# Kernel optimization log

Hardware: AMD Instinct MI355X
Metric: run time of the kernel (lower is better)

The kernel has to match this reference:

```python
import jax, jax.numpy as jnp
import numpy as np

H = 16  # num_heads
B, N, M, D = 4, 512, 2048, 1024
FF = 4096  # mlp_ratio * D
LN_EPS = 1e-5


def _ln(x, g, b):
    m = x.mean(-1, keepdims=True)
    v = ((x - m) ** 2).mean(-1, keepdims=True)
    return (x - m) * jax.lax.rsqrt(v + LN_EPS) * g + b


def _attn(q_in, k_in, v_in, wq, bq, wk, bk, wv, bv, wp, bp):
    b, n, d = q_in.shape
    m = k_in.shape[1]
    hd = d // H
    scale = hd ** -0.5
    q = (q_in @ wq + bq).reshape(b, n, H, hd) * scale
    k = (k_in @ wk + bk).reshape(b, m, H, hd)
    v = (v_in @ wv + bv).reshape(b, m, H, hd)
    attn = jax.nn.softmax(jnp.einsum('bnhd,bmhd->bhnm', q, k), axis=-1)
    out = jnp.einsum('bhnm,bmhd->bnhd', attn, v).reshape(b, n, d)
    return out @ wp + bp


def setup_inputs() -> dict:
    key = jax.random.key(0)
    ks = iter(jax.random.split(key, 32))
    rnd = lambda shape: jax.random.normal(next(ks), shape, dtype=jnp.float32)
    w = lambda *shape: rnd(shape) * 0.02
    inp = {
        'state': rnd((B, N, D)),
        'patches': rnd((B, M, D)),
        'patches_pos_embed': rnd((B, M, D)),
        'state_query': rnd((B, N, D)),
    }
    for p in ('ca', 'sa'):
        inp[f'{p}_wq'] = w(D, D); inp[f'{p}_bq'] = jnp.zeros((D,), jnp.float32)
        inp[f'{p}_wk'] = w(D, D); inp[f'{p}_bk'] = jnp.zeros((D,), jnp.float32)
        inp[f'{p}_wv'] = w(D, D); inp[f'{p}_bv'] = jnp.zeros((D,), jnp.float32)
        inp[f'{p}_wp'] = w(D, D); inp[f'{p}_bp'] = jnp.zeros((D,), jnp.float32)
    inp['w1'] = w(D, FF); inp['b1'] = jnp.zeros((FF,), jnp.float32)
    inp['w2'] = w(FF, D); inp['b2'] = jnp.zeros((D,), jnp.float32)
    for i in (1, 2, 3):
        inp[f'n{i}_g'] = jnp.ones((D,), jnp.float32)
        inp[f'n{i}_b'] = jnp.zeros((D,), jnp.float32)
        inp[f'ls{i}'] = jnp.full((D,), 1e-5, jnp.float32)
    return inp


def reference(state, patches, patches_pos_embed, state_query,
              ca_wq, ca_bq, ca_wk, ca_bk, ca_wv, ca_bv, ca_wp, ca_bp,
              sa_wq, sa_bq, sa_wk, sa_bk, sa_wv, sa_bv, sa_wp, sa_bp,
              w1, b1, w2, b2,
              n1_g, n1_b, n2_g, n2_b, n3_g, n3_b,
              ls1, ls2, ls3):
    # pre-norm path of TransformerLayer.forward_pre (dropouts/drop_path = 0)
    state = state + state_query
    kv = patches + patches_pos_embed
    cross = _attn(_ln(state, n1_g, n1_b), kv, patches,
                  ca_wq, ca_bq, ca_wk, ca_bk, ca_wv, ca_bv, ca_wp, ca_bp)
    state = state + cross * ls1
    ns = _ln(state, n2_g, n2_b)
    selfa = _attn(ns, ns, ns,
                  sa_wq, sa_bq, sa_wk, sa_bk, sa_wv, sa_bv, sa_wp, sa_bp)
    state = state + selfa * ls2
    h = jax.nn.gelu(_ln(state, n3_g, n3_b) @ w1 + b1)
    return state + (h @ w2 + b2) * ls3
```

## Files before the change

### kernel.cpp

```cpp
#include <hip/hip_runtime.h>

#define DEV __device__ __forceinline__

typedef __bf16 bf16x8 __attribute__((ext_vector_type(8)));
typedef float f32x4 __attribute__((ext_vector_type(4)));

DEV unsigned short f2bf(float f) {
  __bf16 h = (__bf16)f;
  return __builtin_bit_cast(unsigned short, h);
}
DEV unsigned int cvtpk(float lo, float hi) {
  unsigned int r;
  asm("v_cvt_pk_bf16_f32 %0, %1, %2" : "=v"(r) : "v"(lo), "v"(hi));
  return r;
}

DEV void gload16(const void* g, void* l) {
  __builtin_amdgcn_global_load_lds(
      (const __attribute__((address_space(1))) unsigned int*)g,
      (__attribute__((address_space(3))) unsigned int*)l, 16, 0, 0);
}

DEV void tconv64_body(const float* __restrict__ W, unsigned short* __restrict__ Wt,
                      int K, int N, int bx, int by) {
  __shared__ float tile[64][65];
  const int t = threadIdx.x;
  const int rr = t >> 4;
  const int cc = (t & 15) * 4;
#pragma unroll
  for (int it = 0; it < 4; it++) {
    float4 v = *reinterpret_cast<const float4*>(
        &W[(size_t)(by * 64 + it * 16 + rr) * N + bx * 64 + cc]);
    tile[it * 16 + rr][cc] = v.x;
    tile[it * 16 + rr][cc + 1] = v.y;
    tile[it * 16 + rr][cc + 2] = v.z;
    tile[it * 16 + rr][cc + 3] = v.w;
  }
  __syncthreads();
  const int nr = t >> 3;
  const int kc = (t & 7) * 8;
#pragma unroll
  for (int it = 0; it < 2; it++) {
    const int n = it * 32 + nr;
    uint4 o;
    o.x = cvtpk(tile[kc + 0][n], tile[kc + 1][n]);
    o.y = cvtpk(tile[kc + 2][n], tile[kc + 3][n]);
    o.z = cvtpk(tile[kc + 4][n], tile[kc + 5][n]);
    o.w = cvtpk(tile[kc + 6][n], tile[kc + 7][n]);
    *reinterpret_cast<uint4*>(&Wt[(size_t)(bx * 64 + n) * K + by * 64 + kc]) = o;
  }
}

DEV void add_ln_body(const float* __restrict__ a, const float* b, float* x0_out,
                     unsigned short* __restrict__ y, const float* __restrict__ gam,
                     const float* __restrict__ bet, int row) {
  const int t = threadIdx.x;
  const int c = t * 4;
  const size_t base = (size_t)row * 1024 + c;
  float4 v = *reinterpret_cast<const float4*>(a + base);
  if (b) {
    float4 v2 = *reinterpret_cast<const float4*>(b + base);
    v.x += v2.x; v.y += v2.y; v.z += v2.z; v.w += v2.w;
  }
  if (x0_out) *reinterpret_cast<float4*>(x0_out + base) = v;
  float s = v.x + v.y + v.z + v.w;
  float sq = v.x * v.x + v.y * v.y + v.z * v.z + v.w * v.w;
#pragma unroll
  for (int o = 32; o > 0; o >>= 1) {
    s += __shfl_xor(s, o);
    sq += __shfl_xor(sq, o);
  }
  __shared__ float ps[4], pq[4];
  const int w = t >> 6;
  if ((t & 63) == 0) { ps[w] = s; pq[w] = sq; }
  __syncthreads();
  s = ps[0] + ps[1] + ps[2] + ps[3];
  sq = pq[0] + pq[1] + pq[2] + pq[3];
  const float mean = s * (1.f / 1024.f);
  const float var = sq * (1.f / 1024.f) - mean * mean;
  const float rstd = rsqrtf(var + 1e-5f);
  float4 gv = *reinterpret_cast<const float4*>(gam + c);
  float4 bv = *reinterpret_cast<const float4*>(bet + c);
  uint2 o2;
  o2.x = cvtpk((v.x - mean) * rstd * gv.x + bv.x, (v.y - mean) * rstd * gv.y + bv.y);
  o2.y = cvtpk((v.z - mean) * rstd * gv.z + bv.z, (v.w - mean) * rstd * gv.w + bv.w);
  *reinterpret_cast<uint2*>(y + base) = o2;
}

DEV void kvcast_body(const float* __restrict__ p, const float* __restrict__ pe,
                     unsigned short* __restrict__ kvo, unsigned short* __restrict__ po,
                     int bid) {
  const size_t i = ((size_t)bid * 256 + threadIdx.x) * 4;
  float4 a = *reinterpret_cast<const float4*>(p + i);
  float4 b = *reinterpret_cast<const float4*>(pe + i);
  uint2 kv2, p2;
  kv2.x = cvtpk(a.x + b.x, a.y + b.y);
  kv2.y = cvtpk(a.z + b.z, a.w + b.w);
  p2.x = cvtpk(a.x, a.y);
  p2.y = cvtpk(a.z, a.w);
  *reinterpret_cast<uint2*>(kvo + i) = kv2;
  *reinterpret_cast<uint2*>(po + i) = p2;
}

struct Pre {
  const float* sqw[8]; unsigned short* sqd[8];
  const float* w1; unsigned short* w1t;
  const float* w2; unsigned short* w2t;
  const float* state; const float* squery; float* stateF; unsigned short* lnB;
  const float* n1_g; const float* n1_b;
  const float* patches; const float* ppe; unsigned short* kvB; unsigned short* patB;
  const float* bq; const float* bk; const float* bv; float* bqkv;
};
__global__ __launch_bounds__(256) void prelude_kernel(Pre p) {
  const int bid = blockIdx.x;
  if (bid < 8192) {
    kvcast_body(p.patches, p.ppe, p.kvB, p.patB, bid);
  } else if (bid < 10240) {
    const int i = bid - 8192;
    const int m = i >> 8, wi = i & 255;
    tconv64_body(p.sqw[m], p.sqd[m], 1024, 1024, wi & 15, wi >> 4);
  } else if (bid < 11264) {
    const int i = bid - 10240;
    tconv64_body(p.w1, p.w1t, 1024, 4096, i & 63, i >> 6);
  } else if (bid < 12288) {
    const int i = bid - 11264;
    tconv64_body(p.w2, p.w2t, 4096, 1024, i & 15, i >> 4);
  } else if (bid < 14336) {
    add_ln_body(p.state, p.squery, p.stateF, p.lnB, p.n1_g, p.n1_b, bid - 12288);
  } else {
    const int i = (bid - 14336) * 256 + threadIdx.x;
    p.bqkv[i] = i < 1024 ? p.bq[i] : (i < 2048 ? p.bk[i - 1024] : p.bv[i - 2048]);
  }
}

__global__ __launch_bounds__(256) void add_ln_kernel(
    const float* __restrict__ a, const float* b, float* x0_out,
    unsigned short* __restrict__ y, const float* __restrict__ gam,
    const float* __restrict__ bet) {
  add_ln_body(a, b, x0_out, y, gam, bet, blockIdx.x);
}

DEV void xcd_swizzle(int gx, int gy, int& bx, int& by, int& bz) {
  const int gxy = gx * gy;
  const int nwg = gxy * gridDim.z;
  const int orig = (blockIdx.z * gy + blockIdx.y) * gx + blockIdx.x;
  const int q = nwg >> 3, r = nwg & 7;
  const int xcd = orig & 7;
  int wgid = (xcd < r ? xcd * (q + 1) : r * (q + 1) + (xcd - r) * q) + (orig >> 3);
  bz = wgid / gxy;
  wgid -= bz * gxy;
  if (gy >= gx) { by = wgid / gx; bx = wgid - by * gx; }
  else          { bx = wgid / gy; by = wgid - bx * gy; }
}

template <int BM, int BN>
DEV void gemm_core(const unsigned short* __restrict__ A,
                   const unsigned short* __restrict__ Bt,
                   unsigned short* As, unsigned short* Bs,
                   int brow, int bcol, int K, int lda, int koff,
                   f32x4 (&acc)[BM / 32][BN / 32]) {
  constexpr int WM = BM / 32, WN = BN / 32;
  const int t = threadIdx.x;
  const int lane = t & 63, w = t >> 6;
  const int wr = w >> 1, wc = w & 1;
  const int g = lane >> 4, lr = lane & 15;
  const int srow = lane >> 2, scol = (lane & 3) * 8;

  auto stage = [&](int buf, int k0) {
#pragma unroll
    for (int i = 0; i < BM / 64; i++) {
      const int r0 = (i * 4 + w) * 16;
      gload16(A + (size_t)(brow + r0 + srow) * lda + koff + k0 + scol,
              &As[buf * BM * 32 + r0 * 32]);
    }
#pragma unroll
    for (int i = 0; i < BN / 64; i++) {
      const int r0 = (i * 4 + w) * 16;
      gload16(Bt + (size_t)(bcol + r0 + srow) * lda + koff + k0 + scol,
              &Bs[buf * BN * 32 + r0 * 32]);
    }
  };

  stage(0, 0);
  const int nk = K / 32;
  int cur = 0;
  for (int kt = 0; kt < nk; kt++) {
    __syncthreads();
    if (kt + 1 < nk) stage(cur ^ 1, (kt + 1) * 32);
    bf16x8 af[WM], bfr[WN];
#pragma unroll
    for (int m = 0; m < WM; m++)
      af[m] = *reinterpret_cast<const bf16x8*>(
          &As[cur * BM * 32 + (wr * (BM / 2) + m * 16 + lr) * 32 + g * 8]);
#pragma unroll
    for (int n = 0; n < WN; n++)
      bfr[n] = *reinterpret_cast<const bf16x8*>(
          &Bs[cur * BN * 32 + (wc * (BN / 2) + n * 16 + lr) * 32 + g * 8]);
    __builtin_amdgcn_s_setprio(1);
#pragma unroll
    for (int m = 0; m < WM; m++)
#pragma unroll
      for (int n = 0; n < WN; n++)
        acc[m][n] = __builtin_amdgcn_mfma_f32_16x16x32_bf16(af[m], bfr[n], acc[m][n], 0, 0, 0);
    __builtin_amdgcn_s_setprio(0);
    cur ^= 1;
  }
}

template <int BM, int BN>
DEV void epilogue_vT(f32x4 (&acc)[BM / 32][BN / 32], unsigned short* smem,
                     unsigned short* __restrict__ vT, const float* __restrict__ bias,
                     int brow, int bcol, int vcol0, int vNk, int rpb) {
  constexpr int WM = BM / 32, WN = BN / 32;
  constexpr int LDT = 136;
  const int t = threadIdx.x, lane = t & 63, w = t >> 6;
  const int wr = w >> 1, wc = w & 1;
  const int g = lane >> 4, lr = lane & 15;
  __syncthreads();
#pragma unroll
  for (int m = 0; m < WM; m++) {
    const int row0 = wr * (BM / 2) + m * 16 + g * 4;
#pragma unroll
    for (int n = 0; n < WN; n++) {
      const int cc = wc * (BN / 2) + n * 16 + lr;
      const float bv = bias[bcol + cc];
      uint2 pk;
      pk.x = cvtpk(acc[m][n][0] + bv, acc[m][n][1] + bv);
      pk.y = cvtpk(acc[m][n][2] + bv, acc[m][n][3] + bv);
      *reinterpret_cast<uint2*>(&smem[cc * LDT + row0]) = pk;
    }
  }
  __syncthreads();
  const int b = brow / rpb;
  const int kvb = brow % rpb;
  constexpr int ITERS = BM * BN / (256 * 8);
#pragma unroll
  for (int it = 0; it < ITERS; it++) {
    const int idx = it * 256 + t;
    const int cc = idx / (BM / 8);
    const int ch = idx % (BM / 8);
    const int dg = bcol + cc - vcol0;
    const int h = dg >> 6, d = dg & 63;
    uint4 v = *reinterpret_cast<uint4*>(&smem[cc * LDT + ch * 8]);
    *reinterpret_cast<uint4*>(
        &vT[((size_t)(b * 16 + h) * 64 + d) * vNk + kvb + ch * 8]) = v;
  }
}

template <int EPI, int BM, int BN>
__global__ __launch_bounds__(256) void gemm_kernel(
    const unsigned short* __restrict__ A, const unsigned short* __restrict__ Bt,
    const float* __restrict__ bias, const float* resid,
    const float* __restrict__ ls, void* outp, int M, int N, int K, int lda,
    unsigned short* vT, int vcol0, int vNk, int rpb) {
  constexpr int WM = BM / 32;
  constexpr int WN = BN / 32;
  constexpr int STG = 2 * BM * 32 + 2 * BN * 32;
  constexpr int TRN = BN * 136;
  constexpr int SME = (EPI == 5 && TRN > STG) ? TRN : STG;
  __shared__ __align__(16) unsigned short smem[SME];
  unsigned short* As = smem;
  unsigned short* Bs = smem + 2 * BM * 32;
  const int t = threadIdx.x;
  const int lane = t & 63, w = t >> 6;
  const int wr = w >> 1, wc = w & 1;
  const int g = lane >> 4, lr = lane & 15;

  int bx, by, bz;
  xcd_swizzle(gridDim.x, gridDim.y, bx, by, bz);
  const int brow = by * BM, bcol = bx * BN;

  f32x4 acc[WM][WN] = {};
  gemm_core<BM, BN>(A, Bt, As, Bs, brow, bcol, K, lda, bz * K, acc);

  if (EPI == 5 && bcol >= vcol0) {
    epilogue_vT<BM, BN>(acc, smem, vT, bias, brow, bcol, vcol0, vNk, rpb);
    return;
  }

#pragma unroll
  for (int m = 0; m < WM; m++) {
    const int row0 = brow + wr * (BM / 2) + m * 16 + g * 4;
#pragma unroll
    for (int n = 0; n < WN; n++) {
      const int col = bcol + wc * (BN / 2) + n * 16 + lr;
      const float bv = (EPI == 4) ? 0.f : bias[col];
#pragma unroll
      for (int r = 0; r < 4; r++) {
        const float v = acc[m][n][r] + bv;
        const size_t idx = (size_t)(row0 + r) * N + col;
        if (EPI == 0 || EPI == 5) {
          ((unsigned short*)outp)[idx] = f2bf(v);
        } else if (EPI == 2) {
          ((float*)outp)[idx] = resid[idx] + v * ls[col];
        } else if (EPI == 3) {
          const float tth = tanhf(0.7978845608028654f * (v + 0.044715f * v * v * v));
          ((unsigned short*)outp)[idx] = f2bf(0.5f * v * (1.f + tth));
        } else {
          ((float*)outp)[(size_t)bz * M * N + idx] = v;
        }
      }
    }
  }
}

struct G3 {
  const unsigned short* A[3]; const unsigned short* Bt[3];
  const float* bias[3]; unsigned short* out[3]; int ecum[3];
  unsigned short* vT; int vNk; int rpb;
};
__global__ __launch_bounds__(256) void gemm3_kernel(G3 p, int N, int K) {
  constexpr int BM = 128, BN = 128, WM = BM / 32, WN = BN / 32;
  constexpr int STG = 2 * BM * 32 + 2 * BN * 32;
  constexpr int TRN = BN * 136;
  constexpr int SME = (TRN > STG) ? TRN : STG;
  __shared__ __align__(16) unsigned short smem[SME];
  unsigned short* As = smem;
  unsigned short* Bs = smem + 2 * BM * 32;
  const int t = threadIdx.x;
  const int lane = t & 63, w = t >> 6;
  const int wr = w >> 1, wc = w & 1;
  const int g = lane >> 4, lr = lane & 15;

  int bx, by, bz;
  xcd_swizzle(gridDim.x, gridDim.y, bx, by, bz);
  const int s = (by >= p.ecum[0]) + (by >= p.ecum[1]);
  const int byloc = by - (s ? p.ecum[s - 1] : 0);
  const unsigned short* A = p.A[s];
  const unsigned short* Bt = p.Bt[s];
  const float* bias = p.bias[s];
  const int brow = byloc * BM, bcol = bx * BN;

  f32x4 acc[WM][WN] = {};
  gemm_core<BM, BN>(A, Bt, As, Bs, brow, bcol, K, K, 0, acc);

  if (s == 2) {
    epilogue_vT<BM, BN>(acc, smem, p.vT, bias, brow, bcol, 0, p.vNk, p.rpb);
    return;
  }
  unsigned short* outp = p.out[s];
#pragma unroll
  for (int m = 0; m < WM; m++) {
    const int row0 = brow + wr * (BM / 2) + m * 16 + g * 4;
#pragma unroll
    for (int n = 0; n < WN; n++) {
      const int col = bcol + wc * (BN / 2) + n * 16 + lr;
      const float bv = bias[col];
#pragma unroll
      for (int r = 0; r < 4; r++)
        outp[(size_t)(row0 + r) * N + col] = f2bf(acc[m][n][r] + bv);
    }
  }
}

__global__ __launch_bounds__(256) void splitk_red_kernel(
    const float* __restrict__ p, const float* __restrict__ bias,
    const float* __restrict__ resid, const float* __restrict__ ls,
    float* __restrict__ out) {
  const size_t i = ((size_t)blockIdx.x * 256 + threadIdx.x) * 4;
  const int c = (int)(i & 1023);
  float4 a = *reinterpret_cast<const float4*>(p + i);
  float4 b = *reinterpret_cast<const float4*>(p + 2048ull * 1024 + i);
  float4 rv = *reinterpret_cast<const float4*>(resid + i);
  float4 bb = *reinterpret_cast<const float4*>(bias + c);
  float4 lv = *reinterpret_cast<const float4*>(ls + c);
  float4 o;
  o.x = rv.x + (a.x + b.x + bb.x) * lv.x;
  o.y = rv.y + (a.y + b.y + bb.y) * lv.y;
  o.z = rv.z + (a.z + b.z + bb.z) * lv.z;
  o.w = rv.w + (a.w + b.w + bb.w) * lv.w;
  *reinterpret_cast<float4*>(out + i) = o;
}

__global__ __launch_bounds__(512) void attn_kernel(
    const unsigned short* __restrict__ Q, const unsigned short* __restrict__ Kp,
    const unsigned short* __restrict__ vT, unsigned short* __restrict__ O,
    int RSq, int RSk, int Nq, int Nk, float k2) {
  __shared__ __align__(16) unsigned short Ks[2][128 * 72];
  __shared__ __align__(16) unsigned short Vs[2][64 * 136];
  __shared__ __align__(16) unsigned short Ps[128 * 136];
  const int t = threadIdx.x, lane = t & 63, w = t >> 6;
  const int qt = blockIdx.y, h = blockIdx.x & 15, b = blockIdx.x >> 4;
  const int g = lane >> 4, lr = lane & 15;
  const int ksrow = t >> 2, kscol = (t & 3) * 16;
  const int vsrow = t >> 3, vscol = (t & 7) * 16;

  uint4 qr[2];
  {
    const unsigned short* qp = Q + (size_t)(b * Nq + qt * 128 + w * 16 + lr) * RSq + h * 64 + g * 8;
    qr[0] = *reinterpret_cast<const uint4*>(qp);
    qr[1] = *reinterpret_cast<const uint4*>(qp + 32);
  }
  float m_i = -1e30f, l_i = 0.f;
  f32x4 acc_o[4] = {};

  auto kaddr = [&](int kv0) {
    return reinterpret_cast<const uint4*>(
        Kp + (size_t)(b * Nk + kv0 + ksrow) * RSk + h * 64 + kscol);
  };
  auto vaddr = [&](int kv0) {
    return reinterpret_cast<const uint4*>(
        vT + ((size_t)(b * 16 + h) * 64 + vsrow) * Nk + kv0 + vscol);
  };

  uint4 kr0 = kaddr(0)[0], kr1 = kaddr(0)[1];
  uint4 vr0 = vaddr(0)[0], vr1 = vaddr(0)[1];

  int cur = 0;
  for (int kv0 = 0; kv0 < Nk; kv0 += 128) {
    *reinterpret_cast<uint4*>(&Ks[cur][ksrow * 72 + kscol]) = kr0;
    *reinterpret_cast<uint4*>(&Ks[cur][ksrow * 72 + kscol + 8]) = kr1;
    *reinterpret_cast<uint4*>(&Vs[cur][vsrow * 136 + vscol]) = vr0;
    *reinterpret_cast<uint4*>(&Vs[cur][vsrow * 136 + vscol + 8]) = vr1;
    __syncthreads();
    if (kv0 + 128 < Nk) {
      kr0 = kaddr(kv0 + 128)[0]; kr1 = kaddr(kv0 + 128)[1];
      vr0 = vaddr(kv0 + 128)[0]; vr1 = vaddr(kv0 + 128)[1];
    }

    f32x4 accs[8] = {};
    __builtin_amdgcn_s_setprio(1);
#pragma unroll
    for (int d0 = 0; d0 < 64; d0 += 32) {
      bf16x8 qf = __builtin_bit_cast(bf16x8, qr[d0 >> 5]);
#pragma unroll
      for (int m = 0; m < 8; m++) {
        bf16x8 kf = *reinterpret_cast<const bf16x8*>(&Ks[cur][(m * 16 + lr) * 72 + d0 + g * 8]);
        accs[m] = __builtin_amdgcn_mfma_f32_16x16x32_bf16(kf, qf, accs[m], 0, 0, 0);
      }
    }
    __builtin_amdgcn_s_setprio(0);
    float pmax = -1e30f;
#pragma unroll
    for (int m = 0; m < 8; m++)
#pragma unroll
      for (int r = 0; r < 4; r++) pmax = fmaxf(pmax, accs[m][r]);
    pmax = fmaxf(pmax, __shfl_xor(pmax, 16));
    pmax = fmaxf(pmax, __shfl_xor(pmax, 32));
    const float pm2 = pmax * k2;
    if (!__all(pm2 <= m_i + 8.f)) {
      const float m_new = fmaxf(m_i, pm2);
      const float corr = exp2f(m_i - m_new);
      m_i = m_new;
      l_i *= corr;
#pragma unroll
      for (int r = 0; r < 4; r++) {
        const float cf = __shfl(corr, g * 4 + r);
#pragma unroll
        for (int n = 0; n < 4; n++) acc_o[n][r] *= cf;
      }
    }
    float psum = 0.f;
#pragma unroll
    for (int m = 0; m < 8; m++) {
      float p0 = exp2f(fmaf(accs[m][0], k2, -m_i));
      float p1 = exp2f(fmaf(accs[m][1], k2, -m_i));
      float p2 = exp2f(fmaf(accs[m][2], k2, -m_i));
      float p3 = exp2f(fmaf(accs[m][3], k2, -m_i));
      psum += p0 + p1 + p2 + p3;
      uint2 pk;
      pk.x = cvtpk(p0, p1);
      pk.y = cvtpk(p2, p3);
      *reinterpret_cast<uint2*>(&Ps[(w * 16 + lr) * 136 + m * 16 + g * 4]) = pk;
    }
    psum += __shfl_xor(psum, 16);
    psum += __shfl_xor(psum, 32);
    l_i += psum;
    __builtin_amdgcn_s_setprio(1);
#pragma unroll
    for (int ks = 0; ks < 4; ks++) {
      bf16x8 pf = *reinterpret_cast<const bf16x8*>(&Ps[(w * 16 + lr) * 136 + ks * 32 + g * 8]);
#pragma unroll
      for (int n = 0; n < 4; n++) {
        bf16x8 vf = *reinterpret_cast<const bf16x8*>(&Vs[cur][(n * 16 + lr) * 136 + ks * 32 + g * 8]);
        acc_o[n] = __builtin_amdgcn_mfma_f32_16x16x32_bf16(pf, vf, acc_o[n], 0, 0, 0);
      }
    }
    __builtin_amdgcn_s_setprio(0);
    cur ^= 1;
  }
#pragma unroll
  for (int r = 0; r < 4; r++) {
    const float li = __shfl(l_i, g * 4 + r);
    const float inv = 1.f / li;
    const int qrow = qt * 128 + w * 16 + g * 4 + r;
#pragma unroll
    for (int n = 0; n < 4; n++)
      O[(size_t)(b * Nq + qrow) * 1024 + h * 64 + n * 16 + lr] = f2bf(acc_o[n][r] * inv);
  }
}

extern "C" void kernel_launch(void* const* d_in, const int* in_sizes, int n_in,
                              void* d_out, int out_size, void* d_ws, size_t ws_size,
                              hipStream_t stream) {
  const float* state = (const float*)d_in[0];
  const float* patches = (const float*)d_in[1];
  const float* ppe = (const float*)d_in[2];
  const float* squery = (const float*)d_in[3];
  const float* ca_wq = (const float*)d_in[4];
  const float* ca_bq = (const float*)d_in[5];
  const float* ca_wk = (const float*)d_in[6];
  const float* ca_bk = (const float*)d_in[7];
  const float* ca_wv = (const float*)d_in[8];
  const float* ca_bv = (const float*)d_in[9];
  const float* ca_wp = (const float*)d_in[10];
  const float* ca_bp = (const float*)d_in[11];
  const float* sa_wq = (const float*)d_in[12];
  const float* sa_bq = (const float*)d_in[13];
  const float* sa_wk = (const float*)d_in[14];
  const float* sa_bk = (const float*)d_in[15];
  const float* sa_wv = (const float*)d_in[16];
  const float* sa_bv = (const float*)d_in[17];
  const float* sa_wp = (const float*)d_in[18];
  const float* sa_bp = (const float*)d_in[19];
  const float* w1 = (const float*)d_in[20];
  const float* b1 = (const float*)d_in[21];
  const float* w2 = (const float*)d_in[22];
  const float* b2 = (const float*)d_in[23];
  const float* n1_g = (const float*)d_in[24];
  const float* n1_b = (const float*)d_in[25];
  const float* ls1 = (const float*)d_in[26];
  const float* n2_g = (const float*)d_in[27];
  const float* n2_b = (const float*)d_in[28];
  const float* ls2 = (const float*)d_in[29];
  const float* n3_g = (const float*)d_in[30];
  const float* n3_b = (const float*)d_in[31];
  const float* ls3 = (const float*)d_in[32];

  char* wsp = (char*)d_ws;
  auto alloc = [&](size_t bytes) {
    void* p = (void*)wsp;
    wsp += (bytes + 255) & ~(size_t)255;
    return p;
  };
  float* stateF = (float*)alloc(2048ull * 1024 * 4);
  unsigned short* lnB = (unsigned short*)alloc(2048ull * 1024 * 2);
  unsigned short* kvB = (unsigned short*)alloc(8192ull * 1024 * 2);
  unsigned short* patB = (unsigned short*)alloc(8192ull * 1024 * 2);
  unsigned short* qB = (unsigned short*)alloc(2048ull * 1024 * 2);
  unsigned short* kB = (unsigned short*)alloc(8192ull * 1024 * 2);
  unsigned short* vB = (unsigned short*)alloc(8192ull * 1024 * 2);
  unsigned short* oB = (unsigned short*)alloc(2048ull * 1024 * 2);
  unsigned short* hB = kvB;
  unsigned short* qkvB = kB;
  unsigned short* vTc = vB;
  unsigned short* vTs = qB;
  float* mlp2p = (float*)patB;
  unsigned short* ca_wqt = (unsigned short*)alloc(1024ull * 1024 * 2);
  unsigned short* ca_wkt = (unsigned short*)alloc(1024ull * 1024 * 2);
  unsigned short* ca_wvt = (unsigned short*)alloc(1024ull * 1024 * 2);
  unsigned short* ca_wpt = (unsigned short*)alloc(1024ull * 1024 * 2);
  unsigned short* sa_wqkvt = (unsigned short*)alloc(3072ull * 1024 * 2);
  unsigned short* sa_wpt = (unsigned short*)alloc(1024ull * 1024 * 2);
  unsigned short* w1t = (unsigned short*)alloc(4096ull * 1024 * 2);
  unsigned short* w2t = (unsigned short*)alloc(4096ull * 1024 * 2);
  float* sa_bqkv = (float*)alloc(3072 * 4);

  Pre pre;
  pre.sqw[0] = ca_wq; pre.sqd[0] = ca_wqt;
  pre.sqw[1] = ca_wk; pre.sqd[1] = ca_wkt;
  pre.sqw[2] = ca_wv; pre.sqd[2] = ca_wvt;
  pre.sqw[3] = ca_wp; pre.sqd[3] = ca_wpt;
  pre.sqw[4] = sa_wq; pre.sqd[4] = sa_wqkvt;
  pre.sqw[5] = sa_wk; pre.sqd[5] = sa_wqkvt + 1024ull * 1024;
  pre.sqw[6] = sa_wv; pre.sqd[6] = sa_wqkvt + 2048ull * 1024;
  pre.sqw[7] = sa_wp; pre.sqd[7] = sa_wpt;
  pre.w1 = w1; pre.w1t = w1t; pre.w2 = w2; pre.w2t = w2t;
  pre.state = state; pre.squery = squery; pre.stateF = stateF; pre.lnB = lnB;
  pre.n1_g = n1_g; pre.n1_b = n1_b;
  pre.patches = patches; pre.ppe = ppe; pre.kvB = kvB; pre.patB = patB;
  pre.bq = sa_bq; pre.bk = sa_bk; pre.bv = sa_bv; pre.bqkv = sa_bqkv;
  prelude_kernel<<<14348, 256, 0, stream>>>(pre);

  const float k2 = 0.125f * 1.4426950408889634f;

  G3 g3;
  g3.A[0] = lnB;  g3.Bt[0] = ca_wqt; g3.bias[0] = ca_bq; g3.out[0] = qB;      g3.ecum[0] = 16;
  g3.A[1] = kvB;  g3.Bt[1] = ca_wkt; g3.bias[1] = ca_bk; g3.out[1] = kB;      g3.ecum[1] = 80;
  g3.A[2] = patB; g3.Bt[2] = ca_wvt; g3.bias[2] = ca_bv; g3.out[2] = nullptr; g3.ecum[2] = 144;
  g3.vT = vTc; g3.vNk = 2048; g3.rpb = 2048;
  gemm3_kernel<<<dim3(8, 144), 256, 0, stream>>>(g3, 1024, 1024);
  attn_kernel<<<dim3(64, 4), 512, 0, stream>>>(qB, kB, vTc, oB, 1024, 1024, 512, 2048, k2);
  gemm_kernel<2, 64, 64><<<dim3(16, 32), 256, 0, stream>>>(oB, ca_wpt, ca_bp, stateF, ls1, stateF, 2048, 1024, 1024, 1024, nullptr, 0, 0, 0);

  add_ln_kernel<<<2048, 256, 0, stream>>>(stateF, nullptr, nullptr, lnB, n2_g, n2_b);
  gemm_kernel<5, 128, 64><<<dim3(48, 16), 256, 0, stream>>>(lnB, sa_wqkvt, sa_bqkv, nullptr, nullptr, qkvB, 2048, 3072, 1024, 1024, vTs, 2048, 512, 512);
  attn_kernel<<<dim3(64, 4), 512, 0, stream>>>(qkvB, qkvB + 1024, vTs, oB, 3072, 3072, 512, 512, k2);
  gemm_kernel<2, 64, 64><<<dim3(16, 32), 256, 0, stream>>>(oB, sa_wpt, sa_bp, stateF, ls2, stateF, 2048, 1024, 1024, 1024, nullptr, 0, 0, 0);

  add_ln_kernel<<<2048, 256, 0, stream>>>(stateF, nullptr, nullptr, lnB, n3_g, n3_b);
  gemm_kernel<3, 128, 128><<<dim3(32, 16), 256, 0, stream>>>(lnB, w1t, b1, nullptr, nullptr, hB, 2048, 4096, 1024, 1024, nullptr, 0, 0, 0);
  gemm_kernel<4, 128, 64><<<dim3(16, 16, 2), 256, 0, stream>>>(hB, w2t, nullptr, nullptr, nullptr, mlp2p, 2048, 1024, 2048, 4096, nullptr, 0, 0, 0);
  splitk_red_kernel<<<2048, 256, 0, stream>>>(mlp2p, b2, stateF, ls3, (float*)d_out);
}
```

Baseline: 284.2 us.

## Shrink attention LDS footprint and batch four kv-cast items per thread

```diff
diff --git a/kernel.cpp b/kernel.cpp
--- a/kernel.cpp
+++ b/kernel.cpp
@@ -87,19 +87,27 @@
   *reinterpret_cast<uint2*>(y + base) = o2;
 }
 
-DEV void kvcast_body(const float* __restrict__ p, const float* __restrict__ pe,
-                     unsigned short* __restrict__ kvo, unsigned short* __restrict__ po,
-                     int bid) {
-  const size_t i = ((size_t)bid * 256 + threadIdx.x) * 4;
-  float4 a = *reinterpret_cast<const float4*>(p + i);
-  float4 b = *reinterpret_cast<const float4*>(pe + i);
-  uint2 kv2, p2;
-  kv2.x = cvtpk(a.x + b.x, a.y + b.y);
-  kv2.y = cvtpk(a.z + b.z, a.w + b.w);
-  p2.x = cvtpk(a.x, a.y);
-  p2.y = cvtpk(a.z, a.w);
-  *reinterpret_cast<uint2*>(kvo + i) = kv2;
-  *reinterpret_cast<uint2*>(po + i) = p2;
+DEV void kvcast_body4(const float* __restrict__ p, const float* __restrict__ pe,
+                      unsigned short* __restrict__ kvo, unsigned short* __restrict__ po,
+                      int bid) {
+  float4 a[4], b[4];
+  size_t idx[4];
+#pragma unroll
+  for (int it = 0; it < 4; it++) {
+    idx[it] = ((size_t)bid * 256 + threadIdx.x + (size_t)it * 524288) * 4;
+    a[it] = *reinterpret_cast<const float4*>(p + idx[it]);
+    b[it] = *reinterpret_cast<const float4*>(pe + idx[it]);
+  }
+#pragma unroll
+  for (int it = 0; it < 4; it++) {
+    uint2 kv2, p2;
+    kv2.x = cvtpk(a[it].x + b[it].x, a[it].y + b[it].y);
+    kv2.y = cvtpk(a[it].z + b[it].z, a[it].w + b[it].w);
+    p2.x = cvtpk(a[it].x, a[it].y);
+    p2.y = cvtpk(a[it].z, a[it].w);
+    *reinterpret_cast<uint2*>(kvo + idx[it]) = kv2;
+    *reinterpret_cast<uint2*>(po + idx[it]) = p2;
+  }
 }
 
 struct Pre {
@@ -113,22 +121,22 @@
 };
 __global__ __launch_bounds__(256) void prelude_kernel(Pre p) {
   const int bid = blockIdx.x;
-  if (bid < 8192) {
-    kvcast_body(p.patches, p.ppe, p.kvB, p.patB, bid);
-  } else if (bid < 10240) {
-    const int i = bid - 8192;
+  if (bid < 2048) {
+    kvcast_body4(p.patches, p.ppe, p.kvB, p.patB, bid);
+  } else if (bid < 4096) {
+    const int i = bid - 2048;
     const int m = i >> 8, wi = i & 255;
     tconv64_body(p.sqw[m], p.sqd[m], 1024, 1024, wi & 15, wi >> 4);
-  } else if (bid < 11264) {
-    const int i = bid - 10240;
+  } else if (bid < 5120) {
+    const int i = bid - 4096;
     tconv64_body(p.w1, p.w1t, 1024, 4096, i & 63, i >> 6);
-  } else if (bid < 12288) {
-    const int i = bid - 11264;
+  } else if (bid < 6144) {
+    const int i = bid - 5120;
     tconv64_body(p.w2, p.w2t, 4096, 1024, i & 15, i >> 4);
-  } else if (bid < 14336) {
-    add_ln_body(p.state, p.squery, p.stateF, p.lnB, p.n1_g, p.n1_b, bid - 12288);
+  } else if (bid < 8192) {
+    add_ln_body(p.state, p.squery, p.stateF, p.lnB, p.n1_g, p.n1_b, bid - 6144);
   } else {
-    const int i = (bid - 14336) * 256 + threadIdx.x;
+    const int i = (bid - 8192) * 256 + threadIdx.x;
     p.bqkv[i] = i < 1024 ? p.bq[i] : (i < 2048 ? p.bk[i - 1024] : p.bv[i - 2048]);
   }
 }
@@ -377,8 +385,8 @@
     const unsigned short* __restrict__ vT, unsigned short* __restrict__ O,
     int RSq, int RSk, int Nq, int Nk, float k2) {
   __shared__ __align__(16) unsigned short Ks[2][128 * 72];
-  __shared__ __align__(16) unsigned short Vs[2][64 * 136];
-  __shared__ __align__(16) unsigned short Ps[128 * 136];
+  __shared__ __align__(16) unsigned short Vs[64 * 136];
+  __shared__ __align__(16) unsigned short Ps[128 * 72];
   const int t = threadIdx.x, lane = t & 63, w = t >> 6;
   const int qt = blockIdx.y, h = blockIdx.x & 15, b = blockIdx.x >> 4;
   const int g = lane >> 4, lr = lane & 15;
@@ -410,8 +418,8 @@
   for (int kv0 = 0; kv0 < Nk; kv0 += 128) {
     *reinterpret_cast<uint4*>(&Ks[cur][ksrow * 72 + kscol]) = kr0;
     *reinterpret_cast<uint4*>(&Ks[cur][ksrow * 72 + kscol + 8]) = kr1;
-    *reinterpret_cast<uint4*>(&Vs[cur][vsrow * 136 + vscol]) = vr0;
-    *reinterpret_cast<uint4*>(&Vs[cur][vsrow * 136 + vscol + 8]) = vr1;
+    *reinterpret_cast<uint4*>(&Vs[vsrow * 136 + vscol]) = vr0;
+    *reinterpret_cast<uint4*>(&Vs[vsrow * 136 + vscol + 8]) = vr1;
     __syncthreads();
     if (kv0 + 128 < Nk) {
       kr0 = kaddr(kv0 + 128)[0]; kr1 = kaddr(kv0 + 128)[1];
@@ -451,6 +459,7 @@
       }
     }
     float psum = 0.f;
+    uint2 pk4[4];
 #pragma unroll
     for (int m = 0; m < 8; m++) {
       float p0 = exp2f(fmaf(accs[m][0], k2, -m_i));
@@ -461,22 +470,40 @@
       uint2 pk;
       pk.x = cvtpk(p0, p1);
       pk.y = cvtpk(p2, p3);
-      *reinterpret_cast<uint2*>(&Ps[(w * 16 + lr) * 136 + m * 16 + g * 4]) = pk;
+      if (m < 4)
+        *reinterpret_cast<uint2*>(&Ps[(w * 16 + lr) * 72 + m * 16 + g * 4]) = pk;
+      else
+        pk4[m - 4] = pk;
     }
     psum += __shfl_xor(psum, 16);
     psum += __shfl_xor(psum, 32);
     l_i += psum;
     __builtin_amdgcn_s_setprio(1);
 #pragma unroll
-    for (int ks = 0; ks < 4; ks++) {
-      bf16x8 pf = *reinterpret_cast<const bf16x8*>(&Ps[(w * 16 + lr) * 136 + ks * 32 + g * 8]);
+    for (int ks = 0; ks < 2; ks++) {
+      bf16x8 pf = *reinterpret_cast<const bf16x8*>(&Ps[(w * 16 + lr) * 72 + ks * 32 + g * 8]);
 #pragma unroll
       for (int n = 0; n < 4; n++) {
-        bf16x8 vf = *reinterpret_cast<const bf16x8*>(&Vs[cur][(n * 16 + lr) * 136 + ks * 32 + g * 8]);
+        bf16x8 vf = *reinterpret_cast<const bf16x8*>(&Vs[(n * 16 + lr) * 136 + ks * 32 + g * 8]);
         acc_o[n] = __builtin_amdgcn_mfma_f32_16x16x32_bf16(pf, vf, acc_o[n], 0, 0, 0);
       }
     }
     __builtin_amdgcn_s_setprio(0);
+#pragma unroll
+    for (int m = 0; m < 4; m++)
+      *reinterpret_cast<uint2*>(&Ps[(w * 16 + lr) * 72 + m * 16 + g * 4]) = pk4[m];
+    __builtin_amdgcn_s_setprio(1);
+#pragma unroll
+    for (int ks = 2; ks < 4; ks++) {
+      bf16x8 pf = *reinterpret_cast<const bf16x8*>(&Ps[(w * 16 + lr) * 72 + (ks - 2) * 32 + g * 8]);
+#pragma unroll
+      for (int n = 0; n < 4; n++) {
+        bf16x8 vf = *reinterpret_cast<const bf16x8*>(&Vs[(n * 16 + lr) * 136 + ks * 32 + g * 8]);
+        acc_o[n] = __builtin_amdgcn_mfma_f32_16x16x32_bf16(pf, vf, acc_o[n], 0, 0, 0);
+      }
+    }
+    __builtin_amdgcn_s_setprio(0);
+    __syncthreads();
     cur ^= 1;
   }
 #pragma unroll
@@ -570,7 +597,7 @@
   pre.n1_g = n1_g; pre.n1_b = n1_b;
   pre.patches = patches; pre.ppe = ppe; pre.kvB = kvB; pre.patB = patB;
   pre.bq = sa_bq; pre.bk = sa_bk; pre.bv = sa_bv; pre.bqkv = sa_bqkv;
-  prelude_kernel<<<14348, 256, 0, stream>>>(pre);
+  prelude_kernel<<<8204, 256, 0, stream>>>(pre);
 
   const float k2 = 0.125f * 1.4426950408889634f;
 
```

Measured after the change: 287.6 us. No clear change (+1.2%).
